# Optimization experiments

Hardware: AMD Instinct MI355X
Metric: run time of the kernel (lower is better)

Reference implementation:

```python
import jax, jax.numpy as jnp
import numpy as np

DIM = 512
HEADS = 8        # MultiHeadAttention default heads=8 (init 'heads' arg actually sets dim_head)
DIM_HEAD = 64    # from AttentionLayers heads=64 passed positionally as dim_head
HIDDEN = HEADS * DIM_HEAD  # 512
EPS = 1e-5


def setup_inputs() -> dict:
    key = jax.random.key(0)
    ks = jax.random.split(key, 8)
    s = 1.0 / np.sqrt(DIM)
    return {
        "x": jax.random.normal(ks[0], (4, 2048, DIM), dtype=jnp.float32),
        "ln_g": jnp.ones((DIM,), dtype=jnp.float32),
        "ln_b": jnp.zeros((DIM,), dtype=jnp.float32),
        "Wq": jax.random.normal(ks[1], (DIM, HIDDEN), dtype=jnp.float32) * s,
        "Wk": jax.random.normal(ks[2], (DIM, HIDDEN), dtype=jnp.float32) * s,
        "Wv": jax.random.normal(ks[3], (DIM, HIDDEN), dtype=jnp.float32) * s,
        "Wo": jax.random.normal(ks[4], (HIDDEN, DIM), dtype=jnp.float32) * s,
        "bo": jnp.zeros((DIM,), dtype=jnp.float32),
    }


def reference(x, ln_g, ln_b, Wq, Wk, Wv, Wo, bo):
    b, n, d = x.shape
    residual = x
    # pre-norm LayerNorm
    mu = jnp.mean(x, axis=-1, keepdims=True)
    var = jnp.mean((x - mu) ** 2, axis=-1, keepdims=True)
    xn = (x - mu) * jax.lax.rsqrt(var + EPS) * ln_g + ln_b
    # QKV projections (no bias), split into heads: [b, s, h, dh]
    q = (xn @ Wq).reshape(b, n, HEADS, DIM_HEAD)
    k = (xn @ Wk).reshape(b, n, HEADS, DIM_HEAD)
    v = (xn @ Wv).reshape(b, n, HEADS, DIM_HEAD)
    scale = HIDDEN ** (-0.5)  # note: scales by hidden_dim, not dim_head (faithful)
    scores = jnp.einsum('bihd,bjhd->bhij', q, k) * scale  # [b,h,i,j] full matrix
    attn = jax.nn.softmax(scores, axis=-1)
    out = jnp.einsum('bhij,bjhd->bihd', attn, v).reshape(b, n, HIDDEN)
    out = out @ Wo + bo
    # residual; the subsequent FFN layer's output is discarded in the source
    return out + residual
```

## Files before the change

kernel.cpp:

```cpp
#include <hip/hip_runtime.h>
#include <hip/hip_bf16.h>

#define DIM 512
#define SEQ 2048
#define BATCH 4
#define NHEADS 8
#define DH 64
#define NROWS (BATCH * SEQ)
#define LN_EPS 1e-5f

typedef __hip_bfloat16 bf16;
typedef __attribute__((ext_vector_type(8))) short short8;
typedef __attribute__((ext_vector_type(4))) float f32x4;

#define MFMA16(a, b, c) __builtin_amdgcn_mfma_f32_16x16x32_bf16((a), (b), (c), 0, 0, 0)

#if __has_builtin(__builtin_amdgcn_exp2f)
#define EXP2(x) __builtin_amdgcn_exp2f(x)
#else
#define EXP2(x) exp2f(x)
#endif

#if defined(__has_builtin)
#if __has_builtin(__builtin_amdgcn_global_load_lds)
#define HAS_GLDS 1
#endif
#endif

__device__ __forceinline__ void glds16(const bf16* g, bf16* l) {
#ifdef HAS_GLDS
  __builtin_amdgcn_global_load_lds((const __attribute__((address_space(1))) void*)g,
                                   (__attribute__((address_space(3))) void*)l, 16, 0, 0);
#else
  *reinterpret_cast<uint4*>(l) = *reinterpret_cast<const uint4*>(g);
#endif
}

#define Q_SCALE_LOG2E 0.06375872f

__global__ void ln_kernel(const float* __restrict__ x, const float* __restrict__ gamma,
                          const float* __restrict__ beta, bf16* __restrict__ xn) {
  const int row = blockIdx.x;
  const int t = threadIdx.x;
  const float2 v = reinterpret_cast<const float2*>(x + (size_t)row * DIM)[t];
  float s = v.x + v.y;
  float ss = v.x * v.x + v.y * v.y;
#pragma unroll
  for (int off = 32; off > 0; off >>= 1) {
    s += __shfl_down(s, off);
    ss += __shfl_down(ss, off);
  }
  __shared__ float red[8];
  __shared__ float stats[2];
  if ((t & 63) == 0) { red[(t >> 6) * 2] = s; red[(t >> 6) * 2 + 1] = ss; }
  __syncthreads();
  if (t == 0) {
    float S = red[0] + red[2] + red[4] + red[6];
    float SS = red[1] + red[3] + red[5] + red[7];
    float mu = S * (1.0f / DIM);
    float var = SS * (1.0f / DIM) - mu * mu;
    stats[0] = mu;
    stats[1] = rsqrtf(var + LN_EPS);
  }
  __syncthreads();
  const float mu = stats[0], rs = stats[1];
  const float2 gg = reinterpret_cast<const float2*>(gamma)[t];
  const float2 bb = reinterpret_cast<const float2*>(beta)[t];
  __hip_bfloat162 o;
  o.x = __float2bfloat16((v.x - mu) * rs * gg.x + bb.x);
  o.y = __float2bfloat16((v.y - mu) * rs * gg.y + bb.y);
  reinterpret_cast<__hip_bfloat162*>(xn + (size_t)row * DIM)[t] = o;
}

__global__ void wt_all_kernel(const float* __restrict__ Wq, const float* __restrict__ Wk,
                              const float* __restrict__ Wv, const float* __restrict__ Wo,
                              bf16* __restrict__ Wt) {
  const int z = blockIdx.z;
  const float* __restrict__ W = (z == 0) ? Wq : (z == 1) ? Wk : (z == 2) ? Wv : Wo;
  const float scale = (z == 0) ? Q_SCALE_LOG2E : 1.0f;
  bf16* __restrict__ dst = Wt + (size_t)z * DIM * DIM;
  __shared__ float tile[32][33];
  const int bx = blockIdx.x, by = blockIdx.y;
  const int tx = threadIdx.x & 31, ty = threadIdx.x >> 5;
#pragma unroll
  for (int i = 0; i < 32; i += 8)
    tile[ty + i][tx] = W[(size_t)(by * 32 + ty + i) * DIM + bx * 32 + tx];
  __syncthreads();
#pragma unroll
  for (int i = 0; i < 32; i += 8)
    dst[(size_t)(bx * 32 + ty + i) * DIM + by * 32 + tx] =
        __float2bfloat16(tile[tx][ty + i] * scale);
}

__launch_bounds__(256, 2)
__global__ void gemm_qkv_kernel(const bf16* __restrict__ A, const bf16* __restrict__ Bt,
                                bf16* __restrict__ qo, bf16* __restrict__ ko,
                                bf16* __restrict__ vo) {
  const int m0 = blockIdx.x * 128, n0g = blockIdx.y * 128;
  __shared__ __align__(16) bf16 sA[128 * 32];
  __shared__ __align__(16) bf16 sB[128 * 32];
  const int t = threadIdx.x, w = t >> 6, l = t & 63;
  const int r = l & 15, g = l >> 4;
  const int wm = w >> 1, wn = w & 1;
  const int crow = w * 32 + (l >> 2);
  const int ccol = (l & 3) * 8;
  const bf16* gA = A + (size_t)(m0 + crow) * DIM + ccol;
  const bf16* gB = Bt + (size_t)(n0g + crow) * DIM + ccol;
  bf16* lA = sA + w * 1024 + l * 8;
  bf16* lB = sB + w * 1024 + l * 8;
  f32x4 acc[4][4] = {};
  for (int k0 = 0; k0 < DIM; k0 += 32) {
    glds16(gA + k0, lA);
    glds16(gA + 16 * DIM + k0, lA + 512);
    glds16(gB + k0, lB);
    glds16(gB + 16 * DIM + k0, lB + 512);
    __syncthreads();
    short8 af[4], bfv[4];
#pragma unroll
    for (int i = 0; i < 4; i++)
      af[i] = *reinterpret_cast<const short8*>(&sA[(wm * 64 + i * 16 + r) * 32 + g * 8]);
#pragma unroll
    for (int j = 0; j < 4; j++)
      bfv[j] = *reinterpret_cast<const short8*>(&sB[(wn * 64 + j * 16 + r) * 32 + g * 8]);
#pragma unroll
    for (int i = 0; i < 4; i++)
#pragma unroll
      for (int j = 0; j < 4; j++) acc[i][j] = MFMA16(af[i], bfv[j], acc[i][j]);
    __syncthreads();
  }
  const int z = n0g >> 9;
  const int nc0 = (n0g & 511) + wn * 64;
  bf16* __restrict__ outp = (z == 0) ? qo : (z == 1) ? ko : vo;
#pragma unroll
  for (int i = 0; i < 4; i++)
#pragma unroll
    for (int j = 0; j < 4; j++)
#pragma unroll
      for (int reg = 0; reg < 4; reg++) {
        const int m = m0 + wm * 64 + i * 16 + g * 4 + reg;
        const int col = nc0 + j * 16 + r;
        outp[(size_t)m * DIM + col] = __float2bfloat16(acc[i][j][reg]);
      }
}

__global__ void vtrans_kernel(const bf16* __restrict__ v, bf16* __restrict__ vt) {
  __shared__ __align__(16) bf16 sT[64][72];
  const int s0 = blockIdx.x * 64, d0 = blockIdx.y * 64, b = blockIdx.z;
  const int t = threadIdx.x;
  const int row = t >> 2, col = (t & 3) * 8;
  const bf16* src = v + ((size_t)(b * SEQ) + s0 + row) * DIM + d0 + col;
  reinterpret_cast<uint4&>(sT[row][col]) = *reinterpret_cast<const uint4*>(src);
  reinterpret_cast<uint4&>(sT[row][col + 32]) = *reinterpret_cast<const uint4*>(src + 32);
  __syncthreads();
  const int drow = t >> 2, jcol = (t & 3) * 8;
  bf16 tmp[8], tmp2[8];
#pragma unroll
  for (int jj = 0; jj < 8; jj++) tmp[jj] = sT[jcol + jj][drow];
#pragma unroll
  for (int jj = 0; jj < 8; jj++) tmp2[jj] = sT[jcol + 32 + jj][drow];
  bf16* dst = vt + ((size_t)(b * DIM) + d0 + drow) * SEQ + s0 + jcol;
  *reinterpret_cast<uint4*>(dst) = *reinterpret_cast<const uint4*>(tmp);
  *reinterpret_cast<uint4*>(dst + 32) = *reinterpret_cast<const uint4*>(tmp2);
}

__launch_bounds__(128, 2)
__global__ void attn_kernel(const bf16* __restrict__ q, const bf16* __restrict__ k,
                            const bf16* __restrict__ vt, bf16* __restrict__ ao) {
  const int it = blockIdx.x, bh = blockIdx.y;
  const int b = bh >> 3, h = bh & 7;
  const int t = threadIdx.x, wv = t >> 6, l = t & 63;
  const int r = l & 15, g = l >> 4;
  __shared__ __align__(16) bf16 sK[64 * 64];
  __shared__ __align__(16) bf16 sV[64 * 64];
  __shared__ __align__(16) bf16 sP[2][2][16][68];
  const int i0 = it * 64 + wv * 32;
  const bf16* qp = q + ((size_t)(b * SEQ) + i0 + r) * DIM + h * DH;
  short8 qf[2][2];
#pragma unroll
  for (int s = 0; s < 2; s++)
#pragma unroll
    for (int kc = 0; kc < 2; kc++)
      qf[s][kc] = *reinterpret_cast<const short8*>(qp + s * 16 * DIM + kc * 32 + g * 8);
  f32x4 oacc[2][4] = {};
  float lrow[2][4] = {{0.f, 0.f, 0.f, 0.f}, {0.f, 0.f, 0.f, 0.f}};
  const int srow8 = l >> 3;
  const int u = ((l & 7) - srow8) & 7;
  const bf16* kg = k + ((size_t)(b * SEQ) + wv * 32 + srow8) * DIM + h * DH + u * 8;
  const bf16* vg = vt + ((size_t)(b * DIM) + h * DH + wv * 32 + srow8) * SEQ + u * 8;
  bf16* lK = sK + (wv * 4) * 512 + l * 8;
  bf16* lV = sV + (wv * 4) * 512 + l * 8;
  const int e0 = 64 * r + 8 * ((g + r) & 7);
  const int e1 = 64 * r + 8 * ((4 + g + r) & 7);
  const int NT = SEQ / 64;
  for (int jt = 0; jt < NT; jt++) {
#pragma unroll
    for (int cc = 0; cc < 4; cc++) {
      glds16(kg + (size_t)(jt * 64 + cc * 8) * DIM, lK + cc * 512);
      glds16(vg + (size_t)(cc * 8) * SEQ + jt * 64, lV + cc * 512);
    }
    __syncthreads();
    f32x4 sc[2][4];
#pragma unroll
    for (int c = 0; c < 4; c++) {
      const short8 kf0 = *reinterpret_cast<const short8*>(sK + 1024 * c + e0);
      const short8 kf1 = *reinterpret_cast<const short8*>(sK + 1024 * c + e1);
#pragma unroll
      for (int s = 0; s < 2; s++) {
        f32x4 a = {0.f, 0.f, 0.f, 0.f};
        a = MFMA16(qf[s][0], kf0, a);
        a = MFMA16(qf[s][1], kf1, a);
        sc[s][c] = a;
      }
    }
#pragma unroll
    for (int s = 0; s < 2; s++)
#pragma unroll
      for (int c = 0; c < 4; c++)
#pragma unroll
        for (int reg = 0; reg < 4; reg++) {
          const float pe = EXP2(sc[s][c][reg]);
          lrow[s][reg] += pe;
          sP[wv][s][g * 4 + reg][c * 16 + r] = __float2bfloat16(pe);
        }
#pragma unroll
    for (int kc2 = 0; kc2 < 2; kc2++) {
      short8 pf[2];
#pragma unroll
      for (int s = 0; s < 2; s++)
        pf[s] = *reinterpret_cast<const short8*>(&sP[wv][s][r][kc2 * 32 + g * 8]);
      const int ev = (kc2 == 0) ? e0 : e1;
#pragma unroll
      for (int dt = 0; dt < 4; dt++) {
        const short8 vf = *reinterpret_cast<const short8*>(sV + 1024 * dt + ev);
#pragma unroll
        for (int s = 0; s < 2; s++) oacc[s][dt] = MFMA16(pf[s], vf, oacc[s][dt]);
      }
    }
    __syncthreads();
  }
#pragma unroll
  for (int s = 0; s < 2; s++)
#pragma unroll
    for (int reg = 0; reg < 4; reg++) {
      float sum = lrow[s][reg];
#pragma unroll
      for (int off = 1; off < 16; off <<= 1) sum += __shfl_xor(sum, off);
      lrow[s][reg] = 1.0f / sum;
    }
#pragma unroll
  for (int s = 0; s < 2; s++)
#pragma unroll
    for (int dt = 0; dt < 4; dt++)
#pragma unroll
      for (int reg = 0; reg < 4; reg++) {
        const int i = i0 + s * 16 + g * 4 + reg;
        const int d = dt * 16 + r;
        ao[((size_t)(b * SEQ) + i) * DIM + h * DH + d] =
            __float2bfloat16(oacc[s][dt][reg] * lrow[s][reg]);
      }
}

__launch_bounds__(256, 2)
__global__ void gemm_proj_kernel(const bf16* __restrict__ A, const bf16* __restrict__ Bt,
                                 const float* __restrict__ bo, const float* __restrict__ x,
                                 float* __restrict__ out) {
  const int m0 = blockIdx.x * 128, n0 = blockIdx.y * 128;
  __shared__ __align__(16) bf16 sA[128 * 32];
  __shared__ __align__(16) bf16 sB[128 * 32];
  const int t = threadIdx.x, w = t >> 6, l = t & 63;
  const int r = l & 15, g = l >> 4;
  const int wm = w >> 1, wn = w & 1;
  const int crow = w * 32 + (l >> 2);
  const int ccol = (l & 3) * 8;
  const bf16* gA = A + (size_t)(m0 + crow) * DIM + ccol;
  const bf16* gB = Bt + (size_t)(n0 + crow) * DIM + ccol;
  bf16* lA = sA + w * 1024 + l * 8;
  bf16* lB = sB + w * 1024 + l * 8;
  f32x4 acc[4][4] = {};
  for (int k0 = 0; k0 < DIM; k0 += 32) {
    glds16(gA + k0, lA);
    glds16(gA + 16 * DIM + k0, lA + 512);
    glds16(gB + k0, lB);
    glds16(gB + 16 * DIM + k0, lB + 512);
    __syncthreads();
    short8 af[4], bfv[4];
#pragma unroll
    for (int i = 0; i < 4; i++)
      af[i] = *reinterpret_cast<const short8*>(&sA[(wm * 64 + i * 16 + r) * 32 + g * 8]);
#pragma unroll
    for (int j = 0; j < 4; j++)
      bfv[j] = *reinterpret_cast<const short8*>(&sB[(wn * 64 + j * 16 + r) * 32 + g * 8]);
#pragma unroll
    for (int i = 0; i < 4; i++)
#pragma unroll
      for (int j = 0; j < 4; j++) acc[i][j] = MFMA16(af[i], bfv[j], acc[i][j]);
    __syncthreads();
  }
#pragma unroll
  for (int i = 0; i < 4; i++)
#pragma unroll
    for (int j = 0; j < 4; j++)
#pragma unroll
      for (int reg = 0; reg < 4; reg++) {
        const int m = m0 + wm * 64 + i * 16 + g * 4 + reg;
        const int col = n0 + wn * 64 + j * 16 + r;
        out[(size_t)m * DIM + col] = acc[i][j][reg] + bo[col] + x[(size_t)m * DIM + col];
      }
}

extern "C" void kernel_launch(void* const* d_in, const int* in_sizes, int n_in,
                              void* d_out, int out_size, void* d_ws, size_t ws_size,
                              hipStream_t stream) {
  (void)in_sizes; (void)n_in; (void)out_size; (void)ws_size;
  const float* x    = (const float*)d_in[0];
  const float* ln_g = (const float*)d_in[1];
  const float* ln_b = (const float*)d_in[2];
  const float* Wq   = (const float*)d_in[3];
  const float* Wk   = (const float*)d_in[4];
  const float* Wv   = (const float*)d_in[5];
  const float* Wo   = (const float*)d_in[6];
  const float* bo   = (const float*)d_in[7];
  float* out = (float*)d_out;
  char* ws = (char*)d_ws;
  bf16* xn  = (bf16*)(ws);
  bf16* vtb = (bf16*)(ws);
  bf16* wt  = (bf16*)(ws + (8u << 20));
  bf16* qb  = (bf16*)(ws + (10u << 20));
  bf16* kb  = (bf16*)(ws + (18u << 20));
  bf16* vb  = (bf16*)(ws + (26u << 20));
  bf16* aob = (bf16*)(ws + (34u << 20));

  ln_kernel<<<NROWS, 256, 0, stream>>>(x, ln_g, ln_b, xn);
  wt_all_kernel<<<dim3(16, 16, 4), 256, 0, stream>>>(Wq, Wk, Wv, Wo, wt);
  gemm_qkv_kernel<<<dim3(NROWS / 128, (3 * DIM) / 128), 256, 0, stream>>>(xn, wt, qb, kb, vb);
  vtrans_kernel<<<dim3(SEQ / 64, DIM / 64, BATCH), 256, 0, stream>>>(vb, vtb);
  attn_kernel<<<dim3(SEQ / 64, BATCH * NHEADS), 128, 0, stream>>>(qb, kb, vtb, aob);
  gemm_proj_kernel<<<dim3(NROWS / 128, DIM / 128), 256, 0, stream>>>(aob, wt + 3 * DIM * DIM,
                                                                     bo, x, out);
}
```

Before: 188.9 us.

## Double-buffer LDS tiles in GEMMs and attention, narrow projection tile

After: 211.9 us. +12.2%, slower.

```diff
diff --git a/kernel.cpp b/kernel.cpp
--- a/kernel.cpp
+++ b/kernel.cpp
@@ -92,13 +92,13 @@
         __float2bfloat16(tile[tx][ty + i] * scale);
 }
 
-__launch_bounds__(256, 2)
+__launch_bounds__(256, 3)
 __global__ void gemm_qkv_kernel(const bf16* __restrict__ A, const bf16* __restrict__ Bt,
                                 bf16* __restrict__ qo, bf16* __restrict__ ko,
                                 bf16* __restrict__ vo) {
   const int m0 = blockIdx.x * 128, n0g = blockIdx.y * 128;
-  __shared__ __align__(16) bf16 sA[128 * 32];
-  __shared__ __align__(16) bf16 sB[128 * 32];
+  __shared__ __align__(16) bf16 sA[2][128 * 32];
+  __shared__ __align__(16) bf16 sB[2][128 * 32];
   const int t = threadIdx.x, w = t >> 6, l = t & 63;
   const int r = l & 15, g = l >> 4;
   const int wm = w >> 1, wn = w & 1;
@@ -106,27 +106,34 @@
   const int ccol = (l & 3) * 8;
   const bf16* gA = A + (size_t)(m0 + crow) * DIM + ccol;
   const bf16* gB = Bt + (size_t)(n0g + crow) * DIM + ccol;
-  bf16* lA = sA + w * 1024 + l * 8;
-  bf16* lB = sB + w * 1024 + l * 8;
+  const int loff = w * 1024 + l * 8;
   f32x4 acc[4][4] = {};
-  for (int k0 = 0; k0 < DIM; k0 += 32) {
-    glds16(gA + k0, lA);
-    glds16(gA + 16 * DIM + k0, lA + 512);
-    glds16(gB + k0, lB);
-    glds16(gB + 16 * DIM + k0, lB + 512);
+  glds16(gA, sA[0] + loff);
+  glds16(gA + 16 * DIM, sA[0] + loff + 512);
+  glds16(gB, sB[0] + loff);
+  glds16(gB + 16 * DIM, sB[0] + loff + 512);
+  const int NK = DIM / 32;
+  for (int ks = 0; ks < NK; ks++) {
+    const int cur = ks & 1;
     __syncthreads();
+    if (ks + 1 < NK) {
+      const int k0n = (ks + 1) * 32;
+      glds16(gA + k0n, sA[1 - cur] + loff);
+      glds16(gA + 16 * DIM + k0n, sA[1 - cur] + loff + 512);
+      glds16(gB + k0n, sB[1 - cur] + loff);
+      glds16(gB + 16 * DIM + k0n, sB[1 - cur] + loff + 512);
+    }
     short8 af[4], bfv[4];
 #pragma unroll
     for (int i = 0; i < 4; i++)
-      af[i] = *reinterpret_cast<const short8*>(&sA[(wm * 64 + i * 16 + r) * 32 + g * 8]);
+      af[i] = *reinterpret_cast<const short8*>(&sA[cur][(wm * 64 + i * 16 + r) * 32 + g * 8]);
 #pragma unroll
     for (int j = 0; j < 4; j++)
-      bfv[j] = *reinterpret_cast<const short8*>(&sB[(wn * 64 + j * 16 + r) * 32 + g * 8]);
+      bfv[j] = *reinterpret_cast<const short8*>(&sB[cur][(wn * 64 + j * 16 + r) * 32 + g * 8]);
 #pragma unroll
     for (int i = 0; i < 4; i++)
 #pragma unroll
       for (int j = 0; j < 4; j++) acc[i][j] = MFMA16(af[i], bfv[j], acc[i][j]);
-    __syncthreads();
   }
   const int z = n0g >> 9;
   const int nc0 = (n0g & 511) + wn * 64;
@@ -170,8 +177,8 @@
   const int b = bh >> 3, h = bh & 7;
   const int t = threadIdx.x, wv = t >> 6, l = t & 63;
   const int r = l & 15, g = l >> 4;
-  __shared__ __align__(16) bf16 sK[64 * 64];
-  __shared__ __align__(16) bf16 sV[64 * 64];
+  __shared__ __align__(16) bf16 sK[2][64 * 64];
+  __shared__ __align__(16) bf16 sV[2][64 * 64];
   __shared__ __align__(16) bf16 sP[2][2][16][68];
   const int i0 = it * 64 + wv * 32;
   const bf16* qp = q + ((size_t)(b * SEQ) + i0 + r) * DIM + h * DH;
@@ -187,23 +194,31 @@
   const int u = ((l & 7) - srow8) & 7;
   const bf16* kg = k + ((size_t)(b * SEQ) + wv * 32 + srow8) * DIM + h * DH + u * 8;
   const bf16* vg = vt + ((size_t)(b * DIM) + h * DH + wv * 32 + srow8) * SEQ + u * 8;
-  bf16* lK = sK + (wv * 4) * 512 + l * 8;
-  bf16* lV = sV + (wv * 4) * 512 + l * 8;
+  const int loff = (wv * 4) * 512 + l * 8;
   const int e0 = 64 * r + 8 * ((g + r) & 7);
   const int e1 = 64 * r + 8 * ((4 + g + r) & 7);
   const int NT = SEQ / 64;
+#pragma unroll
+  for (int cc = 0; cc < 4; cc++) {
+    glds16(kg + (size_t)(cc * 8) * DIM, sK[0] + loff + cc * 512);
+    glds16(vg + (size_t)(cc * 8) * SEQ, sV[0] + loff + cc * 512);
+  }
   for (int jt = 0; jt < NT; jt++) {
-#pragma unroll
-    for (int cc = 0; cc < 4; cc++) {
-      glds16(kg + (size_t)(jt * 64 + cc * 8) * DIM, lK + cc * 512);
-      glds16(vg + (size_t)(cc * 8) * SEQ + jt * 64, lV + cc * 512);
-    }
+    const int cur = jt & 1;
     __syncthreads();
+    if (jt + 1 < NT) {
+      const int j0n = (jt + 1) * 64;
+#pragma unroll
+      for (int cc = 0; cc < 4; cc++) {
+        glds16(kg + (size_t)(j0n + cc * 8) * DIM, sK[1 - cur] + loff + cc * 512);
+        glds16(vg + (size_t)(cc * 8) * SEQ + j0n, sV[1 - cur] + loff + cc * 512);
+      }
+    }
     f32x4 sc[2][4];
 #pragma unroll
     for (int c = 0; c < 4; c++) {
-      const short8 kf0 = *reinterpret_cast<const short8*>(sK + 1024 * c + e0);
-      const short8 kf1 = *reinterpret_cast<const short8*>(sK + 1024 * c + e1);
+      const short8 kf0 = *reinterpret_cast<const short8*>(sK[cur] + 1024 * c + e0);
+      const short8 kf1 = *reinterpret_cast<const short8*>(sK[cur] + 1024 * c + e1);
 #pragma unroll
       for (int s = 0; s < 2; s++) {
         f32x4 a = {0.f, 0.f, 0.f, 0.f};
@@ -231,12 +246,11 @@
       const int ev = (kc2 == 0) ? e0 : e1;
 #pragma unroll
       for (int dt = 0; dt < 4; dt++) {
-        const short8 vf = *reinterpret_cast<const short8*>(sV + 1024 * dt + ev);
+        const short8 vf = *reinterpret_cast<const short8*>(sV[cur] + 1024 * dt + ev);
 #pragma unroll
         for (int s = 0; s < 2; s++) oacc[s][dt] = MFMA16(pf[s], vf, oacc[s][dt]);
       }
     }
-    __syncthreads();
   }
 #pragma unroll
   for (int s = 0; s < 2; s++)
@@ -264,46 +278,51 @@
 __global__ void gemm_proj_kernel(const bf16* __restrict__ A, const bf16* __restrict__ Bt,
                                  const float* __restrict__ bo, const float* __restrict__ x,
                                  float* __restrict__ out) {
-  const int m0 = blockIdx.x * 128, n0 = blockIdx.y * 128;
-  __shared__ __align__(16) bf16 sA[128 * 32];
-  __shared__ __align__(16) bf16 sB[128 * 32];
+  const int m0 = blockIdx.x * 128, n0 = blockIdx.y * 64;
+  __shared__ __align__(16) bf16 sA[2][128 * 32];
+  __shared__ __align__(16) bf16 sB[2][64 * 32];
   const int t = threadIdx.x, w = t >> 6, l = t & 63;
   const int r = l & 15, g = l >> 4;
   const int wm = w >> 1, wn = w & 1;
-  const int crow = w * 32 + (l >> 2);
-  const int ccol = (l & 3) * 8;
-  const bf16* gA = A + (size_t)(m0 + crow) * DIM + ccol;
-  const bf16* gB = Bt + (size_t)(n0 + crow) * DIM + ccol;
-  bf16* lA = sA + w * 1024 + l * 8;
-  bf16* lB = sB + w * 1024 + l * 8;
-  f32x4 acc[4][4] = {};
-  for (int k0 = 0; k0 < DIM; k0 += 32) {
-    glds16(gA + k0, lA);
-    glds16(gA + 16 * DIM + k0, lA + 512);
-    glds16(gB + k0, lB);
-    glds16(gB + 16 * DIM + k0, lB + 512);
+  const int arow = t >> 2;
+  const int ccol = (t & 3) * 8;
+  const bf16* gA = A + (size_t)(m0 + arow) * DIM + ccol;
+  const bf16* gB = Bt + (size_t)(n0 + arow) * DIM + ccol;
+  const int loff = t * 8;
+  f32x4 acc[4][2] = {};
+  glds16(gA, sA[0] + loff);
+  glds16(gA + 64 * DIM, sA[0] + loff + 2048);
+  glds16(gB, sB[0] + loff);
+  const int NK = DIM / 32;
+  for (int ks = 0; ks < NK; ks++) {
+    const int cur = ks & 1;
     __syncthreads();
-    short8 af[4], bfv[4];
+    if (ks + 1 < NK) {
+      const int k0n = (ks + 1) * 32;
+      glds16(gA + k0n, sA[1 - cur] + loff);
+      glds16(gA + 64 * DIM + k0n, sA[1 - cur] + loff + 2048);
+      glds16(gB + k0n, sB[1 - cur] + loff);
+    }
+    short8 af[4], bfv[2];
 #pragma unroll
     for (int i = 0; i < 4; i++)
-      af[i] = *reinterpret_cast<const short8*>(&sA[(wm * 64 + i * 16 + r) * 32 + g * 8]);
-#pragma unroll
-    for (int j = 0; j < 4; j++)
-      bfv[j] = *reinterpret_cast<const short8*>(&sB[(wn * 64 + j * 16 + r) * 32 + g * 8]);
+      af[i] = *reinterpret_cast<const short8*>(&sA[cur][(wm * 64 + i * 16 + r) * 32 + g * 8]);
+#pragma unroll
+    for (int j = 0; j < 2; j++)
+      bfv[j] = *reinterpret_cast<const short8*>(&sB[cur][(wn * 32 + j * 16 + r) * 32 + g * 8]);
 #pragma unroll
     for (int i = 0; i < 4; i++)
 #pragma unroll
-      for (int j = 0; j < 4; j++) acc[i][j] = MFMA16(af[i], bfv[j], acc[i][j]);
-    __syncthreads();
+      for (int j = 0; j < 2; j++) acc[i][j] = MFMA16(af[i], bfv[j], acc[i][j]);
   }
 #pragma unroll
   for (int i = 0; i < 4; i++)
 #pragma unroll
-    for (int j = 0; j < 4; j++)
+    for (int j = 0; j < 2; j++)
 #pragma unroll
       for (int reg = 0; reg < 4; reg++) {
         const int m = m0 + wm * 64 + i * 16 + g * 4 + reg;
-        const int col = n0 + wn * 64 + j * 16 + r;
+        const int col = n0 + wn * 32 + j * 16 + r;
         out[(size_t)m * DIM + col] = acc[i][j][reg] + bo[col] + x[(size_t)m * DIM + col];
       }
 }
@@ -335,6 +354,6 @@
   gemm_qkv_kernel<<<dim3(NROWS / 128, (3 * DIM) / 128), 256, 0, stream>>>(xn, wt, qb, kb, vb);
   vtrans_kernel<<<dim3(SEQ / 64, DIM / 64, BATCH), 256, 0, stream>>>(vb, vtb);
   attn_kernel<<<dim3(SEQ / 64, BATCH * NHEADS), 128, 0, stream>>>(qb, kb, vtb, aob);
-  gemm_proj_kernel<<<dim3(NROWS / 128, DIM / 128), 256, 0, stream>>>(aob, wt + 3 * DIM * DIM,
-                                                                     bo, x, out);
-}
+  gemm_proj_kernel<<<dim3(NROWS / 128, DIM / 64), 256, 0, stream>>>(aob, wt + 3 * DIM * DIM,
+                                                                    bo, x, out);
+}
```
